# Kernel optimization log

Hardware: AMD Instinct MI355X
Metric: run time of the kernel (lower is better)

## Reference

```python
import jax, jax.numpy as jnp
import numpy as np

HIDDEN = 256
B = 1024
T = 1024
IN_DIM = 2
OUT_DIM = 2
DECAY = 0.8  # integrator decay per step


def setup_inputs() -> dict:
    key = jax.random.key(0)
    k_x, k_win, k_bin, k_wout, k_bout, k_tau = jax.random.split(key, 6)
    x_seq = jax.random.normal(k_x, (B, T, IN_DIM), dtype=jnp.float32)
    # nn.Linear init: U(-1/sqrt(fan_in), 1/sqrt(fan_in))
    lim_in = 1.0 / np.sqrt(IN_DIM)
    lim_out = 1.0 / np.sqrt(HIDDEN)
    W_in = jax.random.uniform(k_win, (HIDDEN, IN_DIM), jnp.float32, -lim_in, lim_in)
    b_in = jax.random.uniform(k_bin, (HIDDEN,), jnp.float32, -lim_in, lim_in)
    W_out = jax.random.uniform(k_wout, (OUT_DIM, HIDDEN), jnp.float32, -lim_out, lim_out)
    b_out = jax.random.uniform(k_bout, (OUT_DIM,), jnp.float32, -lim_out, lim_out)
    tau_m = jax.random.uniform(k_tau, (HIDDEN,), jnp.float32, 0.0, 4.0)
    return {"x_seq": x_seq, "W_in": W_in, "b_in": b_in,
            "W_out": W_out, "b_out": b_out, "tau_m": tau_m}


def reference(x_seq, W_in, b_in, W_out, b_out, tau_m):
    # Precompute input currents for all timesteps with one big GEMM: [B,T,H]
    currents = jnp.einsum('bti,hi->bth', x_seq, W_in) + b_in
    alpha = jax.nn.sigmoid(tau_m)  # [H], constant across time

    v0 = jnp.zeros((x_seq.shape[0], W_in.shape[0]), dtype=x_seq.dtype)
    integ0 = jnp.zeros((x_seq.shape[0], W_out.shape[0]), dtype=x_seq.dtype)

    def step(carry, cur_t):
        v, integ = carry
        v = v * alpha + (1.0 - alpha) * cur_t          # LIF membrane update
        spikes = (v >= 1.0).astype(v.dtype)            # hard threshold
        v = v - spikes                                 # soft reset
        out_current = spikes @ W_out.T + b_out         # [B, 2]
        integ = DECAY * integ + out_current
        return (v, integ), None

    # scan over time axis: currents transposed to [T, B, H]
    (v_f, integ_f), _ = jax.lax.scan(step, (v0, integ0),
                                     jnp.swapaxes(currents, 0, 1))
    return integ_f
```

## Files before the change

### kernel.cpp

```cpp
#include <hip/hip_runtime.h>
#include <math.h>


constexpr int T_STEPS = 1024;
constexpr int HIDDEN  = 256;
constexpr int BLK     = 128;
constexpr int NENT    = T_STEPS / 2;

typedef float f32x2 __attribute__((ext_vector_type(2)));
typedef float f32x4 __attribute__((ext_vector_type(4)));

static __device__ __forceinline__ f32x2 pk_mul(f32x2 a, f32x2 b) {
    f32x2 d; asm("v_pk_mul_f32 %0, %1, %2" : "=v"(d) : "v"(a), "v"(b)); return d;
}
static __device__ __forceinline__ f32x2 pk_add(f32x2 a, f32x2 b) {
    f32x2 d; asm("v_pk_add_f32 %0, %1, %2" : "=v"(d) : "v"(a), "v"(b)); return d;
}
static __device__ __forceinline__ f32x2 pk_fma(f32x2 a, f32x2 b, f32x2 c) {
    f32x2 d; asm("v_pk_fma_f32 %0, %1, %2, %3" : "=v"(d) : "v"(a), "v"(b), "v"(c)); return d;
}
static __device__ __forceinline__ f32x2 pk_mul_bc0s(f32x2 x, f32x2 w) {
    f32x2 d; asm("v_pk_mul_f32 %0, %1, %2 op_sel:[0,0] op_sel_hi:[0,1]"
                 : "=v"(d) : "s"(x), "v"(w)); return d;
}
static __device__ __forceinline__ f32x2 pk_mul_bc1s(f32x2 x, f32x2 w) {
    f32x2 d; asm("v_pk_mul_f32 %0, %1, %2 op_sel:[1,0] op_sel_hi:[1,1]"
                 : "=v"(d) : "s"(x), "v"(w)); return d;
}
static __device__ __forceinline__ float spike_neg(float v) {
    return __builtin_amdgcn_fmed3f(-floorf(v), -1.0f, 0.0f);
}

__global__ __launch_bounds__(BLK) void sfnn_smem_kernel(
    const float* __restrict__ x_seq,
    const float* __restrict__ W_in,
    const float* __restrict__ b_in,
    const float* __restrict__ W_out,
    const float* __restrict__ b_out,
    const float* __restrict__ tau_m,
    float* __restrict__ out)
{
    __shared__ float red[4];

    const int b   = blockIdx.x;
    const int tid = threadIdx.x;
    const int h0  = tid;
    const int h1  = tid + BLK;

    const f32x4* __restrict__ xg =
        reinterpret_cast<const f32x4*>(x_seq) + (size_t)b * NENT;

    f32x2 w0p, w1p, bip, alp, bep, c08;
    w0p.x = W_in[2 * h0];     w0p.y = W_in[2 * h1];
    w1p.x = W_in[2 * h0 + 1]; w1p.y = W_in[2 * h1 + 1];
    bip.x = b_in[h0];         bip.y = b_in[h1];
    alp.x = 1.0f / (1.0f + expf(-tau_m[h0]));
    alp.y = 1.0f / (1.0f + expf(-tau_m[h1]));
    bep.x = 1.0f - alp.x;     bep.y = 1.0f - alp.y;
    c08.x = 0.8f;             c08.y = 0.8f;

    f32x2 v  = {0.0f, 0.0f};
    f32x2 Sn = {0.0f, 0.0f};

    #define LIF_STEP(XP)                                                      \
        {                                                                     \
            f32x2 cur = pk_add(pk_add(pk_mul_bc0s((XP), w0p),                 \
                                      pk_mul_bc1s((XP), w1p)), bip);          \
            v = pk_add(pk_mul(v, alp), pk_mul(bep, cur));                     \
            f32x2 spn;                                                        \
            spn.x = spike_neg(v.x);                                           \
            spn.y = spike_neg(v.y);                                           \
            v  = pk_add(v, spn);                                              \
            Sn = pk_fma(c08, Sn, spn);                                        \
        }
    #define LIF2(Q)                                                           \
        LIF_STEP(__builtin_shufflevector((Q), (Q), 0, 1))                     \
        LIF_STEP(__builtin_shufflevector((Q), (Q), 2, 3))

    f32x4 q0 = xg[0];
    f32x4 q1 = xg[1];
    f32x4 q2 = xg[2];
    f32x4 q3 = xg[3];
    for (int i = 0; i < NENT - 4; i += 4) {
        LIF2(q0) q0 = xg[i + 4];
        LIF2(q1) q1 = xg[i + 5];
        LIF2(q2) q2 = xg[i + 6];
        LIF2(q3) q3 = xg[i + 7];
    }
    LIF2(q0) LIF2(q1) LIF2(q2) LIF2(q3)
    #undef LIF2
    #undef LIF_STEP

    const float Sx = -Sn.x, Sy = -Sn.y;
    float r0 = fmaf(Sy, W_out[h1],          Sx * W_out[h0]);
    float r1 = fmaf(Sy, W_out[HIDDEN + h1], Sx * W_out[HIDDEN + h0]);
    #pragma unroll
    for (int off = 32; off > 0; off >>= 1) {
        r0 += __shfl_xor(r0, off, 64);
        r1 += __shfl_xor(r1, off, 64);
    }
    const int wave = tid >> 6;
    if ((tid & 63) == 0) {
        red[2 * wave]     = r0;
        red[2 * wave + 1] = r1;
    }
    __syncthreads();
    if (tid == 0) {
        const float geo = 5.0f;
        out[2 * b]     = (red[0] + red[2]) + b_out[0] * geo;
        out[2 * b + 1] = (red[1] + red[3]) + b_out[1] * geo;
    }
}

extern "C" void kernel_launch(void* const* d_in, const int* in_sizes, int n_in,
                              void* d_out, int out_size, void* d_ws, size_t ws_size,
                              hipStream_t stream) {
    const float* x_seq = (const float*)d_in[0];
    const float* W_in  = (const float*)d_in[1];
    const float* b_in  = (const float*)d_in[2];
    const float* W_out = (const float*)d_in[3];
    const float* b_out = (const float*)d_in[4];
    const float* tau_m = (const float*)d_in[5];
    float* out = (float*)d_out;

    sfnn_smem_kernel<<<dim3(1024), dim3(BLK), 0, stream>>>(
        x_seq, W_in, b_in, W_out, b_out, tau_m, out);
}
```

Baseline: 57.79 us.

## Stream x_seq via double-buffered scalar s_load_dwordx16 with explicit waitcnt

Result: slower. 60.19 us (+4.2%).

```diff
diff --git a/kernel.cpp b/kernel.cpp
--- a/kernel.cpp
+++ b/kernel.cpp
@@ -5,10 +5,9 @@
 constexpr int T_STEPS = 1024;
 constexpr int HIDDEN  = 256;
 constexpr int BLK     = 128;
-constexpr int NENT    = T_STEPS / 2;
 
-typedef float f32x2 __attribute__((ext_vector_type(2)));
-typedef float f32x4 __attribute__((ext_vector_type(4)));
+typedef float f32x2  __attribute__((ext_vector_type(2)));
+typedef float f32x16 __attribute__((ext_vector_type(16)));
 
 static __device__ __forceinline__ f32x2 pk_mul(f32x2 a, f32x2 b) {
     f32x2 d; asm("v_pk_mul_f32 %0, %1, %2" : "=v"(d) : "v"(a), "v"(b)); return d;
@@ -31,7 +30,7 @@
     return __builtin_amdgcn_fmed3f(-floorf(v), -1.0f, 0.0f);
 }
 
-__global__ __launch_bounds__(BLK) void sfnn_smem_kernel(
+__global__ __launch_bounds__(BLK) void sfnn_pp_kernel(
     const float* __restrict__ x_seq,
     const float* __restrict__ W_in,
     const float* __restrict__ b_in,
@@ -47,8 +46,8 @@
     const int h0  = tid;
     const int h1  = tid + BLK;
 
-    const f32x4* __restrict__ xg =
-        reinterpret_cast<const f32x4*>(x_seq) + (size_t)b * NENT;
+    const unsigned long long xbase =
+        (unsigned long long)(x_seq + (size_t)b * T_STEPS * 2);
 
     f32x2 w0p, w1p, bip, alp, bep, c08;
     w0p.x = W_in[2 * h0];     w0p.y = W_in[2 * h1];
@@ -62,6 +61,13 @@
     f32x2 v  = {0.0f, 0.0f};
     f32x2 Sn = {0.0f, 0.0f};
 
+    #define S_WAIT  asm volatile("s_waitcnt lgkmcnt(0)" ::: "memory");        \
+                    __builtin_amdgcn_sched_barrier(0);
+    #define SB      __builtin_amdgcn_sched_barrier(0);
+    #define SLOAD16(D, SOFF, IMM)                                             \
+        asm volatile("s_load_dwordx16 %0, %1, %2 offset:" #IMM                \
+                     : "=s"(D) : "s"(xbase), "s"(SOFF));
+
     #define LIF_STEP(XP)                                                      \
         {                                                                     \
             f32x2 cur = pk_add(pk_add(pk_mul_bc0s((XP), w0p),                 \
@@ -73,23 +79,54 @@
             v  = pk_add(v, spn);                                              \
             Sn = pk_fma(c08, Sn, spn);                                        \
         }
-    #define LIF2(Q)                                                           \
-        LIF_STEP(__builtin_shufflevector((Q), (Q), 0, 1))                     \
-        LIF_STEP(__builtin_shufflevector((Q), (Q), 2, 3))
+    #define LIF16(G)                                                          \
+        LIF_STEP(__builtin_shufflevector((G), (G), 0, 1))                     \
+        LIF_STEP(__builtin_shufflevector((G), (G), 2, 3))                     \
+        LIF_STEP(__builtin_shufflevector((G), (G), 4, 5))                     \
+        LIF_STEP(__builtin_shufflevector((G), (G), 6, 7))                     \
+        LIF_STEP(__builtin_shufflevector((G), (G), 8, 9))                     \
+        LIF_STEP(__builtin_shufflevector((G), (G), 10, 11))                   \
+        LIF_STEP(__builtin_shufflevector((G), (G), 12, 13))                   \
+        LIF_STEP(__builtin_shufflevector((G), (G), 14, 15))
 
-    f32x4 q0 = xg[0];
-    f32x4 q1 = xg[1];
-    f32x4 q2 = xg[2];
-    f32x4 q3 = xg[3];
-    for (int i = 0; i < NENT - 4; i += 4) {
-        LIF2(q0) q0 = xg[i + 4];
-        LIF2(q1) q1 = xg[i + 5];
-        LIF2(q2) q2 = xg[i + 6];
-        LIF2(q3) q3 = xg[i + 7];
+    f32x16 A0, A1, B0, B1;
+
+    {
+        unsigned z = 0;
+        SLOAD16(A0, z, 0)
+        SLOAD16(A1, z, 64)
     }
-    LIF2(q0) LIF2(q1) LIF2(q2) LIF2(q3)
-    #undef LIF2
+
+    unsigned soff = 128;
+    for (int p = 0; p < 31; ++p) {
+        S_WAIT
+        SLOAD16(B0, soff, 0)
+        SLOAD16(B1, soff, 64)
+        SB
+        LIF16(A0) LIF16(A1)
+        unsigned soff2 = soff + 128;
+        S_WAIT
+        SLOAD16(A0, soff2, 0)
+        SLOAD16(A1, soff2, 64)
+        SB
+        LIF16(B0) LIF16(B1)
+        soff += 256;
+    }
+    {
+        S_WAIT
+        SLOAD16(B0, soff, 0)
+        SLOAD16(B1, soff, 64)
+        SB
+        LIF16(A0) LIF16(A1)
+        S_WAIT
+        SB
+        LIF16(B0) LIF16(B1)
+    }
+    #undef LIF16
     #undef LIF_STEP
+    #undef SLOAD16
+    #undef S_WAIT
+    #undef SB
 
     const float Sx = -Sn.x, Sy = -Sn.y;
     float r0 = fmaf(Sy, W_out[h1],          Sx * W_out[h0]);
@@ -123,6 +160,6 @@
     const float* tau_m = (const float*)d_in[5];
     float* out = (float*)d_out;
 
-    sfnn_smem_kernel<<<dim3(1024), dim3(BLK), 0, stream>>>(
+    sfnn_pp_kernel<<<dim3(1024), dim3(BLK), 0, stream>>>(
         x_seq, W_in, b_in, W_out, b_out, tau_m, out);
 }
```
